# Optimization experiments

Hardware: AMD Instinct MI355X
Metric: run time of the kernel (lower is better)

The kernel has to match this reference:

```python
import jax, jax.numpy as jnp
import numpy as np

EPS = 1e-12  # torch F.normalize clamp_min eps

def _l2_normalize(x):
    n = jnp.linalg.norm(x, axis=-1, keepdims=True)
    return x / jnp.maximum(n, EPS)

def setup_inputs() -> dict:
    key = jax.random.key(0)
    k1, k2 = jax.random.split(key)
    z_e = jax.random.normal(k1, (32, 256, 32, 32), dtype=jnp.float32)
    weight = jax.random.normal(k2, (1024, 256), dtype=jnp.float32)
    return {"z_e": z_e, "weight": weight}

def reference(z_e, weight):
    B, C, H, W = z_e.shape  # C == embedding_dim
    z = jnp.transpose(z_e, (0, 2, 3, 1))            # [B,H,W,C]
    flat = _l2_normalize(z.reshape(-1, C))          # [N,C]
    w_n = _l2_normalize(weight)                     # [K,C]
    # distances = 2 - 2 * <flat, w_n>; computed without grad in original
    dist = 2.0 - 2.0 * jnp.matmul(flat, w_n.T)      # [N,K]
    idx = jnp.argmin(dist, axis=1)                  # [N]
    z_q = w_n[idx].reshape(B, H, W, C)              # gather codebook rows
    z_q = jnp.transpose(z_q, (0, 3, 1, 2))          # [B,C,H,W]
    indices = idx.reshape(B, H, W)
    return z_q, indices
```

## Files before the change

### kernel.cpp

```cpp
#include <hip/hip_runtime.h>


typedef _Float16 half8 __attribute__((ext_vector_type(8)));
typedef float floatx4 __attribute__((ext_vector_type(4)));

#define C_DIM 256
#define K_CODES 1024
#define HW 1024
#define NPIX 32768

#define GLOAD_LDS16(g, l) __builtin_amdgcn_global_load_lds(                    \
    (const __attribute__((address_space(1))) unsigned int*)(g),                \
    (__attribute__((address_space(3))) unsigned int*)(l), 16, 0, 0)

__global__ __launch_bounds__(256) void vq_norm_w(const float* __restrict__ w,
                                                 float* __restrict__ w_nT,
                                                 _Float16* __restrict__ wh,
                                                 _Float16* __restrict__ wl) {
    const int row = blockIdx.x;
    const int t   = threadIdx.x;
    float x = w[row * C_DIM + t];
    float s = x * x;
    #pragma unroll
    for (int off = 32; off > 0; off >>= 1) s += __shfl_down(s, off, 64);
    __shared__ float wsum[4];
    if ((t & 63) == 0) wsum[t >> 6] = s;
    __syncthreads();
    float tot = wsum[0] + wsum[1] + wsum[2] + wsum[3];
    float inv = 1.0f / fmaxf(sqrtf(tot), 1e-12f);
    float y = x * inv;
    w_nT[t * K_CODES + row] = y;
    float ys = 16.0f * y;
    _Float16 hi = (_Float16)ys;
    wh[row * C_DIM + t] = hi;
    wl[row * C_DIM + t] = (_Float16)(ys - (float)hi);
}

__global__ __launch_bounds__(256) void vq_split_z(const float* __restrict__ z,
                                                  _Float16* __restrict__ zh,
                                                  _Float16* __restrict__ zl) {
    __shared__ float tile[64][65];
    const int t  = threadIdx.x;
    const int pt = blockIdx.x;
    const int ct = blockIdx.y;
    const int b  = blockIdx.z;
    const float* zb = z + ((size_t)b * C_DIM + ct * 64) * HW + pt * 64;
    const int rr = t >> 4, pp = (t & 15) * 4;
    #pragma unroll
    for (int pass = 0; pass < 4; pass++) {
        float4 v = *(const float4*)(zb + (size_t)(pass * 16 + rr) * HW + pp);
        *(float4*)&tile[pass * 16 + rr][pp] = v;
    }
    __syncthreads();
    const int pl = t >> 2;
    const size_t pix = (size_t)b * HW + pt * 64 + pl;
    #pragma unroll
    for (int pass = 0; pass < 2; pass++) {
        const int c0 = ((t & 3) + 4 * pass) * 8;
        half8 hi, lo;
        #pragma unroll
        for (int j = 0; j < 8; j++) {
            float x = 4.0f * tile[c0 + j][pl];
            _Float16 h = (_Float16)x;
            hi[j] = h;
            lo[j] = (_Float16)(x - (float)h);
        }
        *(half8*)(zh + pix * C_DIM + ct * 64 + c0) = hi;
        *(half8*)(zl + pix * C_DIM + ct * 64 + c0) = lo;
    }
}

__global__ __launch_bounds__(256, 4) void vq_gemm(
        const _Float16* __restrict__ zh, const _Float16* __restrict__ zl,
        const _Float16* __restrict__ wh, const _Float16* __restrict__ wl,
        float* __restrict__ cand_val, int* __restrict__ cand_idx) {
    __shared__ _Float16 lds[4][4096];
    __shared__ float red_v[128][2];
    __shared__ int   red_i[128][2];

    const int tid  = threadIdx.x;
    const int lane = tid & 63, wave = tid >> 6;
    const int wm = wave >> 1, wn = wave & 1;
    const int quad = lane >> 4, l15 = lane & 15;
    const int m0 = blockIdx.x * 128, n0 = blockIdx.y * 128;

    const _Float16* psrc = (wave == 0) ? zh : (wave == 1) ? zl
                         : (wave == 2) ? wh : wl;
    const int row0 = (wave < 2) ? m0 : n0;
    const _Float16* gbase = psrc + (size_t)(row0 + l15) * C_DIM + quad * 8;
    _Float16* ldsw = &lds[wave][0];

    floatx4 acc[4][4];
    #pragma unroll
    for (int i = 0; i < 4; i++)
        #pragma unroll
        for (int j = 0; j < 4; j++) acc[i][j] = (floatx4){0.f, 0.f, 0.f, 0.f};

    const int afrag = wm * 4, bfrag = wn * 4;

    for (int kt = 0; kt < 8; kt++) {
        __syncthreads();
        const _Float16* g = gbase + kt * 32;
        #pragma unroll
        for (int u = 0; u < 8; u++)
            GLOAD_LDS16(g + u * (16 * C_DIM), ldsw + u * 512);
        __syncthreads();

        half8 ah[4], al[4], bh[4], bl[4];
        #pragma unroll
        for (int i = 0; i < 4; i++) {
            ah[i] = *(const half8*)&lds[0][(afrag + i) * 512 + lane * 8];
            al[i] = *(const half8*)&lds[1][(afrag + i) * 512 + lane * 8];
            bh[i] = *(const half8*)&lds[2][(bfrag + i) * 512 + lane * 8];
            bl[i] = *(const half8*)&lds[3][(bfrag + i) * 512 + lane * 8];
        }
        #pragma unroll
        for (int mi = 0; mi < 4; mi++)
            #pragma unroll
            for (int ni = 0; ni < 4; ni++) {
                acc[mi][ni] = __builtin_amdgcn_mfma_f32_16x16x32_f16(ah[mi], bh[ni], acc[mi][ni], 0, 0, 0);
                acc[mi][ni] = __builtin_amdgcn_mfma_f32_16x16x32_f16(ah[mi], bl[ni], acc[mi][ni], 0, 0, 0);
                acc[mi][ni] = __builtin_amdgcn_mfma_f32_16x16x32_f16(al[mi], bh[ni], acc[mi][ni], 0, 0, 0);
            }
    }

    #pragma unroll
    for (int mi = 0; mi < 4; mi++) {
        #pragma unroll
        for (int r = 0; r < 4; r++) {
            float bv = -__builtin_inff();
            int   bi = 0x7fffffff;
            #pragma unroll
            for (int ni = 0; ni < 4; ni++) {
                float v = acc[mi][ni][r];
                int  ci = n0 + wn * 64 + ni * 16 + l15;
                if (v > bv || (v == bv && ci < bi)) { bv = v; bi = ci; }
            }
            #pragma unroll
            for (int mk = 8; mk; mk >>= 1) {
                float ov = __shfl_xor(bv, mk, 16);
                int   oi = __shfl_xor(bi, mk, 16);
                if (ov > bv || (ov == bv && oi < bi)) { bv = ov; bi = oi; }
            }
            if (l15 == 0) {
                int row = wm * 64 + mi * 16 + quad * 4 + r;
                red_v[row][wn] = bv;
                red_i[row][wn] = bi;
            }
        }
    }
    __syncthreads();
    if (tid < 128) {
        float bv = red_v[tid][0]; int bi = red_i[tid][0];
        float v2 = red_v[tid][1]; int i2 = red_i[tid][1];
        if (v2 > bv || (v2 == bv && i2 < bi)) { bv = v2; bi = i2; }
        const int pix = m0 + tid;
        cand_val[(size_t)pix * 8 + blockIdx.y] = bv;
        cand_idx[(size_t)pix * 8 + blockIdx.y] = bi;
    }
}

__global__ __launch_bounds__(256) void vq_finalize(
        const float* __restrict__ cand_val,
        const int*   __restrict__ cand_idx,
        const float* __restrict__ w_nT,
        float* __restrict__ zq,
        float* __restrict__ idx_out) {
    __shared__ int idx_s[1024];
    const int t  = threadIdx.x;
    const int b  = blockIdx.x;
    const int cg = blockIdx.y;
    #pragma unroll
    for (int q = 0; q < 4; q++) {
        const int p = q * 256 + t;
        const int n = b * 1024 + p;
        const size_t base = (size_t)n * 8;
        float bv = cand_val[base]; int bi = cand_idx[base];
        #pragma unroll
        for (int j = 1; j < 8; j++) {
            float v = cand_val[base + j];
            int   c = cand_idx[base + j];
            if (v > bv || (v == bv && c < bi)) { bv = v; bi = c; }
        }
        idx_s[p] = bi;
        if (cg == 0) idx_out[n] = (float)bi;
    }
    __syncthreads();
    float* zqb = zq + (size_t)b * (C_DIM * HW);
    for (int c = 0; c < 32; c++) {
        const int ch = cg * 32 + c;
        const float* wrow = w_nT + (size_t)ch * K_CODES;
        #pragma unroll
        for (int q = 0; q < 4; q++) {
            const int p = q * 256 + t;
            zqb[(size_t)ch * HW + p] = wrow[idx_s[p]];
        }
    }
}

extern "C" void kernel_launch(void* const* d_in, const int* in_sizes, int n_in,
                              void* d_out, int out_size, void* d_ws, size_t ws_size,
                              hipStream_t stream) {
    const float* z = (const float*)d_in[0];
    const float* w = (const float*)d_in[1];
    float* out     = (float*)d_out;

    char* ws = (char*)d_ws;
    float*    w_nT = (float*)(ws);
    _Float16* wh   = (_Float16*)(ws + (1u << 20));
    _Float16* wl   = (_Float16*)(ws + (3u << 19));
    _Float16* zh   = (_Float16*)(ws + (2u << 20));
    _Float16* zl   = (_Float16*)(ws + 18874368u);
    float*    cval = (float*)(ws + 35651584u);
    int*      cidx = (int*)(ws + 36700160u);

    vq_norm_w<<<K_CODES, 256, 0, stream>>>(w, w_nT, wh, wl);
    vq_split_z<<<dim3(16, 4, 32), 256, 0, stream>>>(z, zh, zl);
    vq_gemm<<<dim3(NPIX / 128, K_CODES / 128), 256, 0, stream>>>(zh, zl, wh, wl, cval, cidx);
    vq_finalize<<<dim3(32, 8), 256, 0, stream>>>(cval, cidx, w_nT, out, out + 8388608);
}
```

Baseline: 189.8 us.

## Fuse z transpose and fp16 hi/lo split into the GEMM A-tile load

Removes the separate vq_split_z kernel, along with its fp16 hi/lo workspace, and has the GEMM read fp32 z directly in its native NCHW layout. Each wave loads float4 rows of channels, does the split in registers and writes transposed half4 pieces into padded LDS (stride 520) to cut bank conflicts. This saves a full write and re-read of 32 MB of split data and one launch. In exchange, every N-tile block (8 per M-tile) reloads and re-splits the same fp32 z tile, and A now goes through a register staging path instead of async global-to-LDS loads.

```diff
diff --git a/kernel.cpp b/kernel.cpp
--- a/kernel.cpp
+++ b/kernel.cpp
@@ -2,12 +2,15 @@
 
 
 typedef _Float16 half8 __attribute__((ext_vector_type(8)));
-typedef float floatx4 __attribute__((ext_vector_type(4)));
+typedef _Float16 half4 __attribute__((ext_vector_type(4)));
+typedef float    floatx4 __attribute__((ext_vector_type(4)));
+typedef float    floatv4 __attribute__((ext_vector_type(4)));
 
 #define C_DIM 256
 #define K_CODES 1024
 #define HW 1024
 #define NPIX 32768
+#define USTR 520
 
 #define GLOAD_LDS16(g, l) __builtin_amdgcn_global_load_lds(                    \
     (const __attribute__((address_space(1))) unsigned int*)(g),                \
@@ -36,45 +39,12 @@
     wl[row * C_DIM + t] = (_Float16)(ys - (float)hi);
 }
 
-__global__ __launch_bounds__(256) void vq_split_z(const float* __restrict__ z,
-                                                  _Float16* __restrict__ zh,
-                                                  _Float16* __restrict__ zl) {
-    __shared__ float tile[64][65];
-    const int t  = threadIdx.x;
-    const int pt = blockIdx.x;
-    const int ct = blockIdx.y;
-    const int b  = blockIdx.z;
-    const float* zb = z + ((size_t)b * C_DIM + ct * 64) * HW + pt * 64;
-    const int rr = t >> 4, pp = (t & 15) * 4;
-    #pragma unroll
-    for (int pass = 0; pass < 4; pass++) {
-        float4 v = *(const float4*)(zb + (size_t)(pass * 16 + rr) * HW + pp);
-        *(float4*)&tile[pass * 16 + rr][pp] = v;
-    }
-    __syncthreads();
-    const int pl = t >> 2;
-    const size_t pix = (size_t)b * HW + pt * 64 + pl;
-    #pragma unroll
-    for (int pass = 0; pass < 2; pass++) {
-        const int c0 = ((t & 3) + 4 * pass) * 8;
-        half8 hi, lo;
-        #pragma unroll
-        for (int j = 0; j < 8; j++) {
-            float x = 4.0f * tile[c0 + j][pl];
-            _Float16 h = (_Float16)x;
-            hi[j] = h;
-            lo[j] = (_Float16)(x - (float)h);
-        }
-        *(half8*)(zh + pix * C_DIM + ct * 64 + c0) = hi;
-        *(half8*)(zl + pix * C_DIM + ct * 64 + c0) = lo;
-    }
-}
-
 __global__ __launch_bounds__(256, 4) void vq_gemm(
-        const _Float16* __restrict__ zh, const _Float16* __restrict__ zl,
+        const float* __restrict__ z,
         const _Float16* __restrict__ wh, const _Float16* __restrict__ wl,
         float* __restrict__ cand_val, int* __restrict__ cand_idx) {
-    __shared__ _Float16 lds[4][4096];
+    __shared__ _Float16 Ah[8 * USTR], Al[8 * USTR];
+    __shared__ _Float16 Bh[8 * USTR], Bl[8 * USTR];
     __shared__ float red_v[128][2];
     __shared__ int   red_i[128][2];
 
@@ -83,12 +53,23 @@
     const int wm = wave >> 1, wn = wave & 1;
     const int quad = lane >> 4, l15 = lane & 15;
     const int m0 = blockIdx.x * 128, n0 = blockIdx.y * 128;
-
-    const _Float16* psrc = (wave == 0) ? zh : (wave == 1) ? zl
-                         : (wave == 2) ? wh : wl;
-    const int row0 = (wave < 2) ? m0 : n0;
-    const _Float16* gbase = psrc + (size_t)(row0 + l15) * C_DIM + quad * 8;
-    _Float16* ldsw = &lds[wave][0];
+    const int b  = m0 >> 10, p0 = m0 & 1023;
+
+    const _Float16* bsrc = (wave < 2) ? wh : wl;
+    _Float16*       bdst = (wave < 2) ? Bh : Bl;
+    const int ub = (wave & 1) * 4;
+    const _Float16* gB[4];
+    _Float16*       lB[4];
+    #pragma unroll
+    for (int i = 0; i < 4; i++) {
+        gB[i] = bsrc + (size_t)(n0 + (ub + i) * 16 + l15) * C_DIM + quad * 8;
+        lB[i] = bdst + (ub + i) * USTR;
+    }
+
+    const int ap = (lane & 31) * 4;
+    const int as = lane >> 5;
+    const int ak = wave * 8 + as * 4;
+    const float* zA = z + ((size_t)b * C_DIM + ak) * HW + p0 + ap;
 
     floatx4 acc[4][4];
     #pragma unroll
@@ -100,19 +81,37 @@
 
     for (int kt = 0; kt < 8; kt++) {
         __syncthreads();
-        const _Float16* g = gbase + kt * 32;
-        #pragma unroll
-        for (int u = 0; u < 8; u++)
-            GLOAD_LDS16(g + u * (16 * C_DIM), ldsw + u * 512);
+        #pragma unroll
+        for (int i = 0; i < 4; i++)
+            GLOAD_LDS16(gB[i] + kt * 32, lB[i]);
+        floatv4 za[4];
+        #pragma unroll
+        for (int r = 0; r < 4; r++)
+            za[r] = *(const floatv4*)(zA + (size_t)(kt * 32 + r) * HW);
+        #pragma unroll
+        for (int i = 0; i < 4; i++) {
+            half4 hv, lv;
+            #pragma unroll
+            for (int r = 0; r < 4; r++) {
+                float xv = 4.0f * za[r][i];
+                _Float16 h = (_Float16)xv;
+                hv[r] = h;
+                lv[r] = (_Float16)(xv - (float)h);
+            }
+            const int p = ap + i;
+            const int aidx = (p >> 4) * USTR + wave * 128 + (p & 15) * 8 + as * 4;
+            *(half4*)&Ah[aidx] = hv;
+            *(half4*)&Al[aidx] = lv;
+        }
         __syncthreads();
 
         half8 ah[4], al[4], bh[4], bl[4];
         #pragma unroll
         for (int i = 0; i < 4; i++) {
-            ah[i] = *(const half8*)&lds[0][(afrag + i) * 512 + lane * 8];
-            al[i] = *(const half8*)&lds[1][(afrag + i) * 512 + lane * 8];
-            bh[i] = *(const half8*)&lds[2][(bfrag + i) * 512 + lane * 8];
-            bl[i] = *(const half8*)&lds[3][(bfrag + i) * 512 + lane * 8];
+            ah[i] = *(const half8*)&Ah[(afrag + i) * USTR + lane * 8];
+            al[i] = *(const half8*)&Al[(afrag + i) * USTR + lane * 8];
+            bh[i] = *(const half8*)&Bh[(bfrag + i) * USTR + lane * 8];
+            bl[i] = *(const half8*)&Bl[(bfrag + i) * USTR + lane * 8];
         }
         #pragma unroll
         for (int mi = 0; mi < 4; mi++)
@@ -209,13 +208,10 @@
     float*    w_nT = (float*)(ws);
     _Float16* wh   = (_Float16*)(ws + (1u << 20));
     _Float16* wl   = (_Float16*)(ws + (3u << 19));
-    _Float16* zh   = (_Float16*)(ws + (2u << 20));
-    _Float16* zl   = (_Float16*)(ws + 18874368u);
-    float*    cval = (float*)(ws + 35651584u);
-    int*      cidx = (int*)(ws + 36700160u);
+    float*    cval = (float*)(ws + (2u << 20));
+    int*      cidx = (int*)(ws + (3u << 20));
 
     vq_norm_w<<<K_CODES, 256, 0, stream>>>(w, w_nT, wh, wl);
-    vq_split_z<<<dim3(16, 4, 32), 256, 0, stream>>>(z, zh, zl);
-    vq_gemm<<<dim3(NPIX / 128, K_CODES / 128), 256, 0, stream>>>(zh, zl, wh, wl, cval, cidx);
+    vq_gemm<<<dim3(NPIX / 128, K_CODES / 128), 256, 0, stream>>>(z, wh, wl, cval, cidx);
     vq_finalize<<<dim3(32, 8), 256, 0, stream>>>(cval, cidx, w_nT, out, out + 8388608);
 }
```

New measurement: 175.4 us. -7.6%, faster.
